# Kernel optimization log

Hardware: AMD Instinct MI355X
Metric: run time of the kernel (lower is better)

## Reference

```python
import jax, jax.numpy as jnp
import numpy as np

N, D, H = 1024, 256, 256


def setup_inputs() -> dict:
    key = jax.random.key(0)
    k1, k2, k3, k4, k5 = jax.random.split(key, 5)
    z = jax.random.normal(k1, (N, D), dtype=jnp.float32)
    # fc1: Linear(2*D, H) -> weight [H, 2*D], bias [H]
    lim1 = 1.0 / np.sqrt(2 * D)
    W1 = jax.random.uniform(k2, (H, 2 * D), dtype=jnp.float32, minval=-lim1, maxval=lim1)
    b1 = jax.random.uniform(k3, (H,), dtype=jnp.float32, minval=-lim1, maxval=lim1)
    # fc2: Linear(H, 1)
    lim2 = 1.0 / np.sqrt(H)
    W2 = jax.random.uniform(k4, (1, H), dtype=jnp.float32, minval=-lim2, maxval=lim2)
    b2 = jax.random.uniform(k5, (1,), dtype=jnp.float32, minval=-lim2, maxval=lim2)
    return {"z": z, "W1": W1, "b1": b1, "W2": W2, "b2": b2}


def reference(z, W1, b1, W2, b2):
    # fc1 applied to concat([row, col]) splits algebraically:
    # cat(row, col) @ W1.T = row @ W1[:, :D].T + col @ W1[:, D:].T
    row_part = z @ W1[:, :D].T            # [N, H] (contribution of row element)
    col_part = z @ W1[:, D:].T            # [N, H] (contribution of col element)
    h = jax.nn.relu(row_part[:, None, :] + col_part[None, :, :] + b1)  # [N, N, H]
    out = jax.nn.sigmoid(jnp.einsum('ijh,h->ij', h, W2[0]) + b2[0])    # [N, N]
    return out
```

## Files before the change

kernel.cpp:

```cpp
#include <hip/hip_runtime.h>

#define NN 1024

typedef __attribute__((ext_vector_type(8))) short short8;
typedef __attribute__((ext_vector_type(4))) float floatx4;
typedef __attribute__((ext_vector_type(4))) unsigned int uint4v;
typedef _Float16 half2v __attribute__((ext_vector_type(2)));

#define R2_OFF   0u
#define CT_OFF   524288u

__device__ __forceinline__ unsigned short f2bf(float x) {
  unsigned u = __float_as_uint(x);
  return (unsigned short)((u + 0x7FFFu + ((u >> 16) & 1u)) >> 16);
}

__device__ __forceinline__ unsigned int pkf16(float a, float b) {
  unsigned int lo = (unsigned int)__builtin_bit_cast(unsigned short, (_Float16)a);
  unsigned int hi = (unsigned int)__builtin_bit_cast(unsigned short, (_Float16)b);
  return lo | (hi << 16);
}

__device__ __forceinline__ void dot2acc(unsigned int a, unsigned int b, float& acc) {
#if __has_builtin(__builtin_amdgcn_fdot2)
  acc = __builtin_amdgcn_fdot2(__builtin_bit_cast(half2v, a),
                               __builtin_bit_cast(half2v, b), acc, false);
#else
  asm("v_dot2_f32_f16 %0, %1, %2, %0" : "+v"(acc) : "v"(a), "v"(b));
#endif
}

__device__ __forceinline__ void pkmaxdot(unsigned int r, unsigned int c,
                                         unsigned int mul, float& acc) {
  unsigned int m;
  asm("v_pk_max_f16 %0, %1, %2" : "=v"(m) : "v"(r), "v"(c));
  dot2acc(m, mul, acc);
}

__global__ __launch_bounds__(256) void k1_fused(const float* __restrict__ z,
    const float* __restrict__ W1, const float* __restrict__ b1,
    const float* __restrict__ W2, char* __restrict__ ws) {
  __shared__ unsigned short zsh[16][272];
  __shared__ unsigned short wsh[4][16][272];
  __shared__ float tile[4][16][17];
  unsigned int* R2 = (unsigned int*)(ws + R2_OFF);
  unsigned int* Ct = (unsigned int*)(ws + CT_OFF);

  const int t = threadIdx.x;
  const int l = t & 63, w = t >> 6;
  const int i0 = blockIdx.x * 16;
  const int tid = blockIdx.y * 4 + w;
  const int q0 = tid * 16;
  const bool topR = q0 < 256;
  const int h0 = q0 & 255;
  const int off = topR ? 0 : 256;

  #pragma unroll
  for (int k = 0; k < 4; ++k) {
    const int f = t + k * 256;
    const int r = f >> 6, c4 = f & 63;
    const float4 v = *(const float4*)(z + (i0 + r) * 256 + c4 * 4);
    ushort4 u;
    u.x = f2bf(v.x); u.y = f2bf(v.y); u.z = f2bf(v.z); u.w = f2bf(v.w);
    *(ushort4*)&zsh[r][c4 * 4] = u;
  }
  #pragma unroll 4
  for (int r = 0; r < 16; ++r) {
    const int h = h0 + r;
    const float wa = fabsf(W2[h]);
    const float sc = topR ? wa : -wa;
    const float4 v = *(const float4*)(W1 + h * 512 + off + l * 4);
    ushort4 u;
    u.x = f2bf(v.x * sc); u.y = f2bf(v.y * sc);
    u.z = f2bf(v.z * sc); u.w = f2bf(v.w * sc);
    *(ushort4*)&wsh[w][r][l * 4] = u;
  }
  __syncthreads();

  floatx4 acc = {0.f, 0.f, 0.f, 0.f};
  const int fr = l & 15, fg = (l >> 4) * 8;
  #pragma unroll
  for (int kk = 0; kk < 8; ++kk) {
    const short8 a  = *(const short8*)&zsh[fr][fg + kk * 32];
    const short8 bb = *(const short8*)&wsh[w][fr][fg + kk * 32];
    acc = __builtin_amdgcn_mfma_f32_16x16x32_bf16(a, bb, acc, 0, 0, 0);
  }

  const int col = l & 15, r0 = (l >> 4) * 4;
  float bias = 0.f;
  if (topR) {
    const int h = q0 + col;
    bias = b1[h] * fabsf(W2[h]);
  }
  #pragma unroll
  for (int q = 0; q < 4; ++q) tile[w][r0 + q][col] = acc[q] + bias;
  __syncthreads();
  const int il = l & 15, g2 = l >> 4;
  if (topR) {
    #pragma unroll
    for (int e = 0; e < 2; ++e) {
      const int qc = g2 * 4 + e * 2;
      const unsigned int pk = pkf16(tile[w][il][qc], tile[w][il][qc + 1]);
      R2[((q0 >> 1) + g2 * 2 + e) * 1024 + (i0 + il)] = pk;
    }
  } else {
    const unsigned int pk0 = pkf16(tile[w][il][g2 * 4 + 0], tile[w][il][g2 * 4 + 1]);
    const unsigned int pk1 = pkf16(tile[w][il][g2 * 4 + 2], tile[w][il][g2 * 4 + 3]);
    const int hpg = ((q0 - 256) >> 3) + (g2 >> 1);
    unsigned int* dst = Ct + (hpg * 1024 + (i0 + il)) * 4 + (g2 & 1) * 2;
    dst[0] = pk0; dst[1] = pk1;
  }
}

__global__ __launch_bounds__(256) void k2_pair(const unsigned int* __restrict__ R2,
    const unsigned int* __restrict__ Ct, const float* __restrict__ W2,
    const float* __restrict__ b2v, float* __restrict__ out) {
  __shared__ unsigned int Rl[128][32];
  __shared__ float part[4][32][65];
  __shared__ float partkv[4][64];
  __shared__ unsigned int MulS[128];
  const int t = threadIdx.x;
  const int lane = t & 63, w = t >> 6;
  const int li = lane >> 4, lj = lane & 15;
  const int i0 = blockIdx.x * 32, j0 = blockIdx.y * 64;

  if (t < 128) {
    const unsigned int s0 = (W2[2 * t]     > 0.f) ? 0x3C00u : 0xBC00u;
    const unsigned int s1 = (W2[2 * t + 1] > 0.f) ? 0x3C00u : 0xBC00u;
    MulS[t] = s0 | (s1 << 16);
  }
  #pragma unroll
  for (int k = 0; k < 16; ++k) {
    const int n = k * 256 + t;
    Rl[n >> 5][n & 31] = R2[(n >> 5) * 1024 + i0 + (n & 31)];
  }
  __syncthreads();

  const int hbase = w * 8;
  float acc[4][4] = {}, acc2[4][4] = {};
  float kvacc[4] = {};

#define LOADC(BUF, MQ, G) do { \
    _Pragma("unroll") \
    for (int jj = 0; jj < 4; ++jj) \
      BUF[jj] = *(const uint4v*)(Ct + (((hbase + (G)) * 1024) + j0 + lj + 16 * jj) * 4); \
    MQ = *(const uint4v*)&MulS[(hbase + (G)) * 4]; \
  } while (0)

#define COMPG(BUF, MQ, G) do { \
    _Pragma("unroll") \
    for (int hp2 = 0; hp2 < 4; ++hp2) { \
      const int hp = (hbase + (G)) * 4 + hp2; \
      const uint4v ra0 = *(const uint4v*)&Rl[hp][li * 8]; \
      const uint4v ra1 = *(const uint4v*)&Rl[hp][li * 8 + 4]; \
      const unsigned int mu = MQ[hp2]; \
      _Pragma("unroll") \
      for (int jj = 0; jj < 4; ++jj) { \
        const unsigned int c = BUF[jj][hp2]; \
        dot2acc(c, mu, kvacc[jj]); \
        _Pragma("unroll") \
        for (int ii = 0; ii < 4; ++ii) pkmaxdot(ra0[ii], c, mu, acc[ii][jj]); \
        _Pragma("unroll") \
        for (int ii = 0; ii < 4; ++ii) pkmaxdot(ra1[ii], c, mu, acc2[ii][jj]); \
      } \
    } \
  } while (0)

  {
    uint4v A[4], B[4], C[4];
    uint4v MA, MB, MC;
    LOADC(A, MA, 0); LOADC(B, MB, 1); LOADC(C, MC, 2);
    COMPG(A, MA, 0); LOADC(A, MA, 3);
    COMPG(B, MB, 1); LOADC(B, MB, 4);
    COMPG(C, MC, 2); LOADC(C, MC, 5);
    COMPG(A, MA, 3); LOADC(A, MA, 6);
    COMPG(B, MB, 4); LOADC(B, MB, 7);
    COMPG(C, MC, 5);
    COMPG(A, MA, 6);
    COMPG(B, MB, 7);
  }
#undef LOADC
#undef COMPG

  #pragma unroll
  for (int ii = 0; ii < 4; ++ii)
    #pragma unroll
    for (int jj = 0; jj < 4; ++jj) {
      part[w][li * 8 + ii][lj + 16 * jj]     = acc[ii][jj];
      part[w][li * 8 + 4 + ii][lj + 16 * jj] = acc2[ii][jj];
    }
  if (li == 0) {
    #pragma unroll
    for (int jj = 0; jj < 4; ++jj) partkv[w][lj + 16 * jj] = kvacc[jj];
  }
  __syncthreads();

  const int jl = t & 63, ib = (t >> 6) * 8;
  const float kvt = partkv[0][jl] + partkv[1][jl] + partkv[2][jl] + partkv[3][jl];
  const float base = b2v[0] - kvt;
  #pragma unroll
  for (int u = 0; u < 8; ++u) {
    const int il = ib + u;
    const float x = part[0][il][jl] + part[1][il][jl] +
                    part[2][il][jl] + part[3][il][jl] + base;
    out[(i0 + il) * NN + j0 + jl] = 1.f / (1.f + __expf(-x));
  }
}

extern "C" void kernel_launch(void* const* d_in, const int* in_sizes, int n_in,
                              void* d_out, int out_size, void* d_ws, size_t ws_size,
                              hipStream_t stream) {
  const float* z  = (const float*)d_in[0];
  const float* W1 = (const float*)d_in[1];
  const float* b1 = (const float*)d_in[2];
  const float* W2 = (const float*)d_in[3];
  const float* b2 = (const float*)d_in[4];
  float* out = (float*)d_out;
  char* ws = (char*)d_ws;

  k1_fused<<<dim3(64, 8), 256, 0, stream>>>(z, W1, b1, W2, ws);
  k2_pair<<<dim3(32, 16), 256, 0, stream>>>(
      (const unsigned int*)(ws + R2_OFF), (const unsigned int*)(ws + CT_OFF),
      W2, b2, out);
}
```

Baseline: 22.99 us.

## Restructure pair kernel: per-wave full-H reduction, drop LDS staging and cross-wave reduce

The pair kernel no longer stages R2 in LDS or splits the hidden dimension across waves with a shared-memory partial-sum reduction. Each wave now owns 4 rows and 64 columns and loops over all 128 packed hidden pairs itself. R values are read as wave-uniform global loads, and the results go straight into the sigmoid output. The grid doubles in x to cover the smaller per-block tile. This removes the LDS traffic, the second barrier and the reduction, at the cost of less register-level reuse (4x1 outputs per thread instead of 8x4), so more Ct loads per output and a longer serial loop per thread.

```diff
diff --git a/kernel.cpp b/kernel.cpp
--- a/kernel.cpp
+++ b/kernel.cpp
@@ -115,96 +115,43 @@
 __global__ __launch_bounds__(256) void k2_pair(const unsigned int* __restrict__ R2,
     const unsigned int* __restrict__ Ct, const float* __restrict__ W2,
     const float* __restrict__ b2v, float* __restrict__ out) {
-  __shared__ unsigned int Rl[128][32];
-  __shared__ float part[4][32][65];
-  __shared__ float partkv[4][64];
   __shared__ unsigned int MulS[128];
   const int t = threadIdx.x;
-  const int lane = t & 63, w = t >> 6;
-  const int li = lane >> 4, lj = lane & 15;
-  const int i0 = blockIdx.x * 32, j0 = blockIdx.y * 64;
-
   if (t < 128) {
     const unsigned int s0 = (W2[2 * t]     > 0.f) ? 0x3C00u : 0xBC00u;
     const unsigned int s1 = (W2[2 * t + 1] > 0.f) ? 0x3C00u : 0xBC00u;
     MulS[t] = s0 | (s1 << 16);
   }
-  #pragma unroll
-  for (int k = 0; k < 16; ++k) {
-    const int n = k * 256 + t;
-    Rl[n >> 5][n & 31] = R2[(n >> 5) * 1024 + i0 + (n & 31)];
-  }
   __syncthreads();
 
-  const int hbase = w * 8;
-  float acc[4][4] = {}, acc2[4][4] = {};
-  float kvacc[4] = {};
+  const int lane = t & 63;
+  const int w = __builtin_amdgcn_readfirstlane(t >> 6);
+  const int i0 = blockIdx.x * 16 + w * 4;
+  const int j  = blockIdx.y * 64 + lane;
 
-#define LOADC(BUF, MQ, G) do { \
-    _Pragma("unroll") \
-    for (int jj = 0; jj < 4; ++jj) \
-      BUF[jj] = *(const uint4v*)(Ct + (((hbase + (G)) * 1024) + j0 + lj + 16 * jj) * 4); \
-    MQ = *(const uint4v*)&MulS[(hbase + (G)) * 4]; \
-  } while (0)
+  float acc0 = 0.f, acc1 = 0.f, acc2 = 0.f, acc3 = 0.f, kv = 0.f;
 
-#define COMPG(BUF, MQ, G) do { \
-    _Pragma("unroll") \
-    for (int hp2 = 0; hp2 < 4; ++hp2) { \
-      const int hp = (hbase + (G)) * 4 + hp2; \
-      const uint4v ra0 = *(const uint4v*)&Rl[hp][li * 8]; \
-      const uint4v ra1 = *(const uint4v*)&Rl[hp][li * 8 + 4]; \
-      const unsigned int mu = MQ[hp2]; \
-      _Pragma("unroll") \
-      for (int jj = 0; jj < 4; ++jj) { \
-        const unsigned int c = BUF[jj][hp2]; \
-        dot2acc(c, mu, kvacc[jj]); \
-        _Pragma("unroll") \
-        for (int ii = 0; ii < 4; ++ii) pkmaxdot(ra0[ii], c, mu, acc[ii][jj]); \
-        _Pragma("unroll") \
-        for (int ii = 0; ii < 4; ++ii) pkmaxdot(ra1[ii], c, mu, acc2[ii][jj]); \
-      } \
-    } \
-  } while (0)
+  #pragma unroll 4
+  for (int g = 0; g < 32; ++g) {
+    const uint4v cc = *(const uint4v*)(Ct + (g * 1024 + j) * 4);
+    const uint4v mq = *(const uint4v*)&MulS[g * 4];
+    #pragma unroll
+    for (int p = 0; p < 4; ++p) {
+      const uint4v ra = *(const uint4v*)(R2 + (g * 4 + p) * 1024 + i0);
+      const unsigned int c = cc[p], mu = mq[p];
+      dot2acc(c, mu, kv);
+      pkmaxdot(ra[0], c, mu, acc0);
+      pkmaxdot(ra[1], c, mu, acc1);
+      pkmaxdot(ra[2], c, mu, acc2);
+      pkmaxdot(ra[3], c, mu, acc3);
+    }
+  }
 
-  {
-    uint4v A[4], B[4], C[4];
-    uint4v MA, MB, MC;
-    LOADC(A, MA, 0); LOADC(B, MB, 1); LOADC(C, MC, 2);
-    COMPG(A, MA, 0); LOADC(A, MA, 3);
-    COMPG(B, MB, 1); LOADC(B, MB, 4);
-    COMPG(C, MC, 2); LOADC(C, MC, 5);
-    COMPG(A, MA, 3); LOADC(A, MA, 6);
-    COMPG(B, MB, 4); LOADC(B, MB, 7);
-    COMPG(C, MC, 5);
-    COMPG(A, MA, 6);
-    COMPG(B, MB, 7);
-  }
-#undef LOADC
-#undef COMPG
-
-  #pragma unroll
-  for (int ii = 0; ii < 4; ++ii)
-    #pragma unroll
-    for (int jj = 0; jj < 4; ++jj) {
-      part[w][li * 8 + ii][lj + 16 * jj]     = acc[ii][jj];
-      part[w][li * 8 + 4 + ii][lj + 16 * jj] = acc2[ii][jj];
-    }
-  if (li == 0) {
-    #pragma unroll
-    for (int jj = 0; jj < 4; ++jj) partkv[w][lj + 16 * jj] = kvacc[jj];
-  }
-  __syncthreads();
-
-  const int jl = t & 63, ib = (t >> 6) * 8;
-  const float kvt = partkv[0][jl] + partkv[1][jl] + partkv[2][jl] + partkv[3][jl];
-  const float base = b2v[0] - kvt;
-  #pragma unroll
-  for (int u = 0; u < 8; ++u) {
-    const int il = ib + u;
-    const float x = part[0][il][jl] + part[1][il][jl] +
-                    part[2][il][jl] + part[3][il][jl] + base;
-    out[(i0 + il) * NN + j0 + jl] = 1.f / (1.f + __expf(-x));
-  }
+  const float base = b2v[0] - kv;
+  out[(i0 + 0) * NN + j] = 1.f / (1.f + __expf(-(acc0 + base)));
+  out[(i0 + 1) * NN + j] = 1.f / (1.f + __expf(-(acc1 + base)));
+  out[(i0 + 2) * NN + j] = 1.f / (1.f + __expf(-(acc2 + base)));
+  out[(i0 + 3) * NN + j] = 1.f / (1.f + __expf(-(acc3 + base)));
 }
 
 extern "C" void kernel_launch(void* const* d_in, const int* in_sizes, int n_in,
@@ -219,7 +166,7 @@
   char* ws = (char*)d_ws;
 
   k1_fused<<<dim3(64, 8), 256, 0, stream>>>(z, W1, b1, W2, ws);
-  k2_pair<<<dim3(32, 16), 256, 0, stream>>>(
+  k2_pair<<<dim3(64, 16), 256, 0, stream>>>(
       (const unsigned int*)(ws + R2_OFF), (const unsigned int*)(ws + CT_OFF),
       W2, b2, out);
 }
```

Result: slower. 26.37 us (+14.7%).
